# Kernel tuning notes

Measured on AMD Instinct MI355X. Metric: run time of the kernel, lower is better.

## Reference

```python
import jax, jax.numpy as jnp
import numpy as np

N_NODES, N_RELS, D, DEG = 100000, 2000, 128, 16
N_EDGES = N_NODES * DEG


def setup_inputs() -> dict:
    key = jax.random.key(0)
    k1, k2, k3, k4, k5 = jax.random.split(key, 5)
    # subject column: sorted and covers every node (tf.math.segment_sum requires
    # sorted segment ids; full coverage avoids 0/0 in the normalization)
    subj = jnp.repeat(jnp.arange(N_NODES, dtype=jnp.int64), DEG)
    rel = jax.random.randint(k1, (N_EDGES,), 0, N_RELS, dtype=jnp.int64)
    obj = jax.random.randint(k2, (N_EDGES,), 0, N_NODES, dtype=jnp.int64)
    triples = jnp.stack([subj, rel, obj], axis=1)[None]  # [1, E, 3]
    features = jax.random.normal(k3, (N_NODES, D), jnp.float32)
    rel_emb = jax.random.normal(k4, (N_RELS, D), jnp.float32)
    attn_kernel = jax.random.normal(k5, (D, 1), jnp.float32) * 0.05  # keep exp() finite
    return {"triples": triples, "features": features, "rel_emb": rel_emb,
            "attn_kernel": attn_kernel}


def reference(triples, features, rel_emb, attn_kernel):
    # single head, 'concat' reduction, linear activation, no bias
    t = jnp.squeeze(triples, 0).astype(jnp.int32)  # [E, 3]
    subj, rel_idx, obj_idx = t[:, 0], t[:, 1], t[:, 2]
    n = features.shape[0]

    obj_embs = features[obj_idx]          # [E, D] gather
    edge_embs = rel_emb[rel_idx]          # [E, D] gather

    # tf.nn.l2_normalize(edge_embs, 1) with eps 1e-12
    edge_n = edge_embs * jax.lax.rsqrt(
        jnp.maximum(jnp.sum(edge_embs * edge_embs, axis=1, keepdims=True), 1e-12))
    # Householder-like reflection (note: projection onto normalized dir, scaled
    # by the UNnormalized edge embedding, exactly as in the source)
    refl = jnp.sum(obj_embs * edge_n, axis=1, keepdims=True) * edge_embs
    obj_embs = obj_embs - 2.0 * refl      # [E, D]

    # per-relation attention logit, gathered per edge
    att_value = jnp.exp(rel_emb @ attn_kernel)[rel_idx]  # [E, 1]

    num = jax.ops.segment_sum(att_value * obj_embs, subj, num_segments=n)  # [N, D]
    den = jax.ops.segment_sum(att_value, subj, num_segments=n)             # [N, 1]
    return num / den
```

## Files before the change

### kernel.cpp

```cpp
#include <hip/hip_runtime.h>
#include <hip/hip_fp16.h>

#define N_NODES 100000
#define N_RELS  2000
#define D       128
#define DEG     16

#define RELWS_BYTES  16384
#define FEAT16_BYTES ((size_t)N_NODES * D * 2)
#define REL16_BYTES  ((size_t)N_RELS * D * 2)
#define WS_NEED      (RELWS_BYTES + FEAT16_BYTES + REL16_BYTES)

static __device__ __forceinline__ __half2 bc_h2(unsigned int u) {
  return __builtin_bit_cast(__half2, u);
}
static __device__ __forceinline__ int bc_i(float f) {
  return __builtin_bit_cast(int, f);
}
static __device__ __forceinline__ float bc_f(int i) {
  return __builtin_bit_cast(float, i);
}

static __device__ __forceinline__ float row16_sum_bcast(float v) {
  v += bc_f(__builtin_amdgcn_update_dpp(0, bc_i(v), 0x111, 0xF, 0xF, false));
  v += bc_f(__builtin_amdgcn_update_dpp(0, bc_i(v), 0x112, 0xF, 0xF, false));
  v += bc_f(__builtin_amdgcn_update_dpp(0, bc_i(v), 0x114, 0xF, 0xF, false));
  v += bc_f(__builtin_amdgcn_update_dpp(0, bc_i(v), 0x118, 0xF, 0xF, false));
  return bc_f(__builtin_amdgcn_ds_swizzle(bc_i(v), 0x1F0));
}

__global__ __launch_bounds__(256) void rel_pre_kernel(
    const float* __restrict__ rel_emb,
    const float* __restrict__ attn,
    float2* __restrict__ relws,
    unsigned int* __restrict__ rel16u) {
  const int wave = threadIdx.x >> 6;
  const int lane = threadIdx.x & 63;
  const int r = blockIdx.x * 4 + wave;
  float2 ev = *(const float2*)(rel_emb + (size_t)r * D + lane * 2);
  float2 av = *(const float2*)(attn + lane * 2);
  rel16u[r * 64 + lane] =
      __builtin_bit_cast(unsigned int, __builtin_amdgcn_cvt_pkrtz(ev.x, ev.y));
  float ss = ev.x * ev.x + ev.y * ev.y;
  float dt = ev.x * av.x + ev.y * av.y;
#pragma unroll
  for (int off = 32; off >= 1; off >>= 1) {
    ss += __shfl_xor(ss, off, 64);
    dt += __shfl_xor(dt, off, 64);
  }
  if (lane == 0) {
    float inv = rsqrtf(fmaxf(ss, 1e-12f));
    relws[r] = make_float2(inv, expf(dt));
  }
}

__global__ __launch_bounds__(256) void cvt_f32_f16_kernel(
    const float* __restrict__ src, uint2* __restrict__ dst) {
  const int i = blockIdx.x * 256 + threadIdx.x;
  float4 v = ((const float4*)src)[i];
  uint2 o;
  o.x = __builtin_bit_cast(unsigned int, __builtin_amdgcn_cvt_pkrtz(v.x, v.y));
  o.y = __builtin_bit_cast(unsigned int, __builtin_amdgcn_cvt_pkrtz(v.z, v.w));
  dst[i] = o;
}

__global__ __launch_bounds__(256) void gat16_kernel(
    const int* __restrict__ triples,
    const unsigned short* __restrict__ feat16,
    const unsigned short* __restrict__ rel16,
    const float2* __restrict__ relws,
    float* __restrict__ out) {
  __shared__ uint2 recs[256];

  const int tid  = threadIdx.x;
  const int s    = tid & 15;
  const int g    = (tid >> 4) & 3;
  const int wave = tid >> 6;
  const int node = blockIdx.x * 16 + wave * 4 + g;

  const int* t = triples + (size_t)node * (DEG * 3);
  const int tr = t[3 * s + 1];
  const int to = t[3 * s + 2];
  const float2 ia = relws[tr];
  const float att = ia.y;
  const float cf  = 2.f * att * ia.x;

  float den = att;
  den += __shfl_xor(den, 1);
  den += __shfl_xor(den, 2);
  den += __shfl_xor(den, 4);
  den += __shfl_xor(den, 8);
  const float rden = 1.f / den;

  recs[tid] = make_uint2(
      (unsigned int)((to << 11) | tr),
      __builtin_bit_cast(unsigned int, __builtin_amdgcn_cvt_pkrtz(att, cf)));
  __syncthreads();

  const int rbase = tid & 0xF0;

  uint4 ofb[8], efb[8];
  unsigned int pacb[8];
#pragma unroll
  for (int i = 0; i < 8; ++i) {
    uint2 r = recs[rbase + i];
    pacb[i] = r.y;
    ofb[i] = *(const uint4*)(feat16 + (size_t)(r.x >> 11) * D + s * 8);
    efb[i] = *(const uint4*)(rel16 + (size_t)(r.x & 2047u) * D + s * 8);
  }

  __half2 acc1[4], acc2[4];
#pragma unroll
  for (int j = 0; j < 4; ++j) {
    acc1[j] = __float2half2_rn(0.f);
    acc2[j] = __float2half2_rn(0.f);
  }

#pragma unroll
  for (int i = 0; i < DEG; ++i) {
    const int j = i & 7;
    const uint4 of = ofb[j];
    const uint4 ef = efb[j];
    const unsigned int ac = pacb[j];
    if (i + 8 < DEG) {
      uint2 r = recs[rbase + i + 8];
      pacb[j] = r.y;
      ofb[j] = *(const uint4*)(feat16 + (size_t)(r.x >> 11) * D + s * 8);
      efb[j] = *(const uint4*)(rel16 + (size_t)(r.x & 2047u) * D + s * 8);
    }

    const __half2 o0 = bc_h2(of.x), o1 = bc_h2(of.y), o2 = bc_h2(of.z), o3 = bc_h2(of.w);
    const __half2 e0 = bc_h2(ef.x), e1 = bc_h2(ef.y), e2 = bc_h2(ef.z), e3 = bc_h2(ef.w);

    __half2 pp = __hmul2(o0, e0);
    pp = __hfma2(o1, e1, pp);
    pp = __hfma2(o2, e2, pp);
    pp = __hfma2(o3, e3, pp);
    const float pd = row16_sum_bcast(__low2float(pp) + __high2float(pp));

    const __half2 h = bc_h2(ac);
    const __half2 att2 = __half2half2(__low2half(h));
    const __half2 c2 = __float2half2_rn(__high2float(h) * pd);

    acc1[0] = __hfma2(att2, o0, acc1[0]);
    acc1[1] = __hfma2(att2, o1, acc1[1]);
    acc1[2] = __hfma2(att2, o2, acc1[2]);
    acc1[3] = __hfma2(att2, o3, acc1[3]);
    acc2[0] = __hfma2(c2, e0, acc2[0]);
    acc2[1] = __hfma2(c2, e1, acc2[1]);
    acc2[2] = __hfma2(c2, e2, acc2[2]);
    acc2[3] = __hfma2(c2, e3, acc2[3]);
  }

  float* op = out + (size_t)node * D + s * 8;
  float4 r0, r1;
  {
    float2 a0 = __half22float2(acc1[0]), b0 = __half22float2(acc2[0]);
    float2 a1 = __half22float2(acc1[1]), b1 = __half22float2(acc2[1]);
    r0.x = (a0.x - b0.x) * rden; r0.y = (a0.y - b0.y) * rden;
    r0.z = (a1.x - b1.x) * rden; r0.w = (a1.y - b1.y) * rden;
    float2 a2 = __half22float2(acc1[2]), b2 = __half22float2(acc2[2]);
    float2 a3 = __half22float2(acc1[3]), b3 = __half22float2(acc2[3]);
    r1.x = (a2.x - b2.x) * rden; r1.y = (a2.y - b2.y) * rden;
    r1.z = (a3.x - b3.x) * rden; r1.w = (a3.y - b3.y) * rden;
  }
  *(float4*)op = r0;
  *(float4*)(op + 4) = r1;
}

__global__ __launch_bounds__(256) void gat_kernel(
    const int* __restrict__ triples,
    const float* __restrict__ features,
    const float* __restrict__ rel_emb,
    const float2* __restrict__ relws,
    float* __restrict__ out) {
  const int wave = threadIdx.x >> 6;
  const int lane = threadIdx.x & 63;
  const int node = blockIdx.x * 4 + wave;
  const int* t = triples + (size_t)node * DEG * 3;
  int tv = (lane < DEG * 3) ? t[lane] : 0;
  float2 acc = make_float2(0.f, 0.f);
  float den = 0.f;
#pragma unroll
  for (int i = 0; i < DEG; ++i) {
    const int rel = __builtin_amdgcn_readfirstlane(__shfl(tv, 3 * i + 1, 64));
    const int obj = __builtin_amdgcn_readfirstlane(__shfl(tv, 3 * i + 2, 64));
    float2 ia = relws[rel];
    float2 ov = *(const float2*)(features + (size_t)obj * D + lane * 2);
    float2 ev = *(const float2*)(rel_emb + (size_t)rel * D + lane * 2);
    float pd = ov.x * ev.x + ov.y * ev.y;
#pragma unroll
    for (int off = 32; off >= 1; off >>= 1) pd += __shfl_xor(pd, off, 64);
    const float c = 2.f * pd * ia.x;
    const float att = ia.y;
    acc.x += att * (ov.x - c * ev.x);
    acc.y += att * (ov.y - c * ev.y);
    den += att;
  }
  const float r = 1.f / den;
  *(float2*)(out + (size_t)node * D + lane * 2) =
      make_float2(acc.x * r, acc.y * r);
}

extern "C" void kernel_launch(void* const* d_in, const int* in_sizes, int n_in,
                              void* d_out, int out_size, void* d_ws, size_t ws_size,
                              hipStream_t stream) {
  const int*   triples  = (const int*)d_in[0];
  const float* features = (const float*)d_in[1];
  const float* rel_emb  = (const float*)d_in[2];
  const float* attn     = (const float*)d_in[3];
  float*       out      = (float*)d_out;

  float2* relws = (float2*)d_ws;

  if (ws_size >= WS_NEED) {
    unsigned short* feat16 = (unsigned short*)((char*)d_ws + RELWS_BYTES);
    unsigned int*   rel16u = (unsigned int*)((char*)d_ws + RELWS_BYTES + FEAT16_BYTES);
    rel_pre_kernel<<<N_RELS / 4, 256, 0, stream>>>(rel_emb, attn, relws, rel16u);
    cvt_f32_f16_kernel<<<(N_NODES * D / 4) / 256, 256, 0, stream>>>(
        features, (uint2*)feat16);
    gat16_kernel<<<N_NODES / 16, 256, 0, stream>>>(
        triples, feat16, (const unsigned short*)rel16u, relws, out);
  } else {
    rel_pre_kernel<<<N_RELS / 4, 256, 0, stream>>>(rel_emb, attn, relws,
                                                   (unsigned int*)d_ws);
    gat_kernel<<<N_NODES / 4, 256, 0, stream>>>(
        triples, features, rel_emb, relws, out);
  }
}
```

Measured before the change: 173.0 us.

## Fuse preprocessing kernels and hand-schedule gather loads with inline asm waitcnts

Measured after the change: 169.4 us. 1.02x faster.

```diff
diff --git a/kernel.cpp b/kernel.cpp
--- a/kernel.cpp
+++ b/kernel.cpp
@@ -10,6 +10,8 @@
 #define FEAT16_BYTES ((size_t)N_NODES * D * 2)
 #define REL16_BYTES  ((size_t)N_RELS * D * 2)
 #define WS_NEED      (RELWS_BYTES + FEAT16_BYTES + REL16_BYTES)
+
+typedef unsigned int u32x4 __attribute__((ext_vector_type(4)));
 
 static __device__ __forceinline__ __half2 bc_h2(unsigned int u) {
   return __builtin_bit_cast(__half2, u);
@@ -27,6 +29,42 @@
   v += bc_f(__builtin_amdgcn_update_dpp(0, bc_i(v), 0x114, 0xF, 0xF, false));
   v += bc_f(__builtin_amdgcn_update_dpp(0, bc_i(v), 0x118, 0xF, 0xF, false));
   return bc_f(__builtin_amdgcn_ds_swizzle(bc_i(v), 0x1F0));
+}
+
+__global__ __launch_bounds__(256) void pre_kernel(
+    const float* __restrict__ features,
+    const float* __restrict__ rel_emb,
+    const float* __restrict__ attn,
+    float2* __restrict__ relws,
+    unsigned int* __restrict__ rel16u,
+    uint2* __restrict__ feat16v) {
+  const int i = blockIdx.x * 256 + threadIdx.x;
+  float4 v = ((const float4*)features)[i];
+  uint2 o;
+  o.x = __builtin_bit_cast(unsigned int, __builtin_amdgcn_cvt_pkrtz(v.x, v.y));
+  o.y = __builtin_bit_cast(unsigned int, __builtin_amdgcn_cvt_pkrtz(v.z, v.w));
+  feat16v[i] = o;
+
+  if (blockIdx.x < N_RELS / 4) {
+    const int wave = threadIdx.x >> 6;
+    const int lane = threadIdx.x & 63;
+    const int r = blockIdx.x * 4 + wave;
+    float2 ev = *(const float2*)(rel_emb + (size_t)r * D + lane * 2);
+    float2 av = *(const float2*)(attn + lane * 2);
+    rel16u[r * 64 + lane] =
+        __builtin_bit_cast(unsigned int, __builtin_amdgcn_cvt_pkrtz(ev.x, ev.y));
+    float ss = ev.x * ev.x + ev.y * ev.y;
+    float dt = ev.x * av.x + ev.y * av.y;
+#pragma unroll
+    for (int off = 32; off >= 1; off >>= 1) {
+      ss += __shfl_xor(ss, off, 64);
+      dt += __shfl_xor(dt, off, 64);
+    }
+    if (lane == 0) {
+      float inv = rsqrtf(fmaxf(ss, 1e-12f));
+      relws[r] = make_float2(inv, expf(dt));
+    }
+  }
 }
 
 __global__ __launch_bounds__(256) void rel_pre_kernel(
@@ -54,15 +92,50 @@
   }
 }
 
-__global__ __launch_bounds__(256) void cvt_f32_f16_kernel(
-    const float* __restrict__ src, uint2* __restrict__ dst) {
-  const int i = blockIdx.x * 256 + threadIdx.x;
-  float4 v = ((const float4*)src)[i];
-  uint2 o;
-  o.x = __builtin_bit_cast(unsigned int, __builtin_amdgcn_cvt_pkrtz(v.x, v.y));
-  o.y = __builtin_bit_cast(unsigned int, __builtin_amdgcn_cvt_pkrtz(v.z, v.w));
-  dst[i] = o;
-}
+
+#define GAT_WAIT(n) asm volatile("s_waitcnt vmcnt(" #n ")")
+
+#define GAT_ISSUE(slot, rx)                                                    \
+  {                                                                            \
+    const unsigned long long fo_ =                                             \
+        (unsigned long long)(feat16 + (size_t)((rx) >> 11) * D + s * 8);       \
+    const unsigned long long fe_ =                                             \
+        (unsigned long long)(rel16 + (size_t)((rx) & 2047u) * D + s * 8);      \
+    asm volatile("global_load_dwordx4 %0, %1, off"                             \
+                 : "=v"(ofb[(slot)]) : "v"(fo_));                              \
+    asm volatile("global_load_dwordx4 %0, %1, off"                             \
+                 : "=v"(efb[(slot)]) : "v"(fe_));                              \
+  }
+
+#define GAT_ITER(i, vmw)                                                       \
+  {                                                                            \
+    GAT_WAIT(vmw);                                                             \
+    __builtin_amdgcn_sched_barrier(0);                                         \
+    const u32x4 of = ofb[(i) & 7];                                             \
+    const u32x4 ef = efb[(i) & 7];                                             \
+    const unsigned int ac = rc[(i)].y;                                         \
+    if constexpr ((i) + 8 < DEG) GAT_ISSUE((i) & 7, rc[(i) + 8].x);            \
+    const __half2 o0 = bc_h2(of.x), o1 = bc_h2(of.y), o2 = bc_h2(of.z),        \
+                  o3 = bc_h2(of.w);                                            \
+    const __half2 e0 = bc_h2(ef.x), e1 = bc_h2(ef.y), e2 = bc_h2(ef.z),        \
+                  e3 = bc_h2(ef.w);                                            \
+    __half2 pp = __hmul2(o0, e0);                                              \
+    pp = __hfma2(o1, e1, pp);                                                  \
+    pp = __hfma2(o2, e2, pp);                                                  \
+    pp = __hfma2(o3, e3, pp);                                                  \
+    const float pd = row16_sum_bcast(__low2float(pp) + __high2float(pp));      \
+    const __half2 h = bc_h2(ac);                                               \
+    const __half2 att2 = __half2half2(__low2half(h));                          \
+    const __half2 c2 = __float2half2_rn(__high2float(h) * pd);                 \
+    acc1[0] = __hfma2(att2, o0, acc1[0]);                                      \
+    acc1[1] = __hfma2(att2, o1, acc1[1]);                                      \
+    acc1[2] = __hfma2(att2, o2, acc1[2]);                                      \
+    acc1[3] = __hfma2(att2, o3, acc1[3]);                                      \
+    acc2[0] = __hfma2(c2, e0, acc2[0]);                                        \
+    acc2[1] = __hfma2(c2, e1, acc2[1]);                                        \
+    acc2[2] = __hfma2(c2, e2, acc2[2]);                                        \
+    acc2[3] = __hfma2(c2, e3, acc2[3]);                                        \
+  }
 
 __global__ __launch_bounds__(256) void gat16_kernel(
     const int* __restrict__ triples,
@@ -99,15 +172,14 @@
 
   const int rbase = tid & 0xF0;
 
-  uint4 ofb[8], efb[8];
-  unsigned int pacb[8];
-#pragma unroll
-  for (int i = 0; i < 8; ++i) {
-    uint2 r = recs[rbase + i];
-    pacb[i] = r.y;
-    ofb[i] = *(const uint4*)(feat16 + (size_t)(r.x >> 11) * D + s * 8);
-    efb[i] = *(const uint4*)(rel16 + (size_t)(r.x & 2047u) * D + s * 8);
-  }
+  uint2 rc[16];
+#pragma unroll
+  for (int i = 0; i < 16; ++i) rc[i] = recs[rbase + i];
+
+  u32x4 ofb[8], efb[8];
+  GAT_WAIT(0);
+#pragma unroll
+  for (int i = 0; i < 8; ++i) GAT_ISSUE(i, rc[i].x);
 
   __half2 acc1[4], acc2[4];
 #pragma unroll
@@ -116,41 +188,10 @@
     acc2[j] = __float2half2_rn(0.f);
   }
 
-#pragma unroll
-  for (int i = 0; i < DEG; ++i) {
-    const int j = i & 7;
-    const uint4 of = ofb[j];
-    const uint4 ef = efb[j];
-    const unsigned int ac = pacb[j];
-    if (i + 8 < DEG) {
-      uint2 r = recs[rbase + i + 8];
-      pacb[j] = r.y;
-      ofb[j] = *(const uint4*)(feat16 + (size_t)(r.x >> 11) * D + s * 8);
-      efb[j] = *(const uint4*)(rel16 + (size_t)(r.x & 2047u) * D + s * 8);
-    }
-
-    const __half2 o0 = bc_h2(of.x), o1 = bc_h2(of.y), o2 = bc_h2(of.z), o3 = bc_h2(of.w);
-    const __half2 e0 = bc_h2(ef.x), e1 = bc_h2(ef.y), e2 = bc_h2(ef.z), e3 = bc_h2(ef.w);
-
-    __half2 pp = __hmul2(o0, e0);
-    pp = __hfma2(o1, e1, pp);
-    pp = __hfma2(o2, e2, pp);
-    pp = __hfma2(o3, e3, pp);
-    const float pd = row16_sum_bcast(__low2float(pp) + __high2float(pp));
-
-    const __half2 h = bc_h2(ac);
-    const __half2 att2 = __half2half2(__low2half(h));
-    const __half2 c2 = __float2half2_rn(__high2float(h) * pd);
-
-    acc1[0] = __hfma2(att2, o0, acc1[0]);
-    acc1[1] = __hfma2(att2, o1, acc1[1]);
-    acc1[2] = __hfma2(att2, o2, acc1[2]);
-    acc1[3] = __hfma2(att2, o3, acc1[3]);
-    acc2[0] = __hfma2(c2, e0, acc2[0]);
-    acc2[1] = __hfma2(c2, e1, acc2[1]);
-    acc2[2] = __hfma2(c2, e2, acc2[2]);
-    acc2[3] = __hfma2(c2, e3, acc2[3]);
-  }
+  GAT_ITER(0, 14)  GAT_ITER(1, 14)  GAT_ITER(2, 14)  GAT_ITER(3, 14)
+  GAT_ITER(4, 14)  GAT_ITER(5, 14)  GAT_ITER(6, 14)  GAT_ITER(7, 14)
+  GAT_ITER(8, 14)  GAT_ITER(9, 12)  GAT_ITER(10, 10) GAT_ITER(11, 8)
+  GAT_ITER(12, 6)  GAT_ITER(13, 4)  GAT_ITER(14, 2)  GAT_ITER(15, 0)
 
   float* op = out + (size_t)node * D + s * 8;
   float4 r0, r1;
@@ -216,9 +257,8 @@
   if (ws_size >= WS_NEED) {
     unsigned short* feat16 = (unsigned short*)((char*)d_ws + RELWS_BYTES);
     unsigned int*   rel16u = (unsigned int*)((char*)d_ws + RELWS_BYTES + FEAT16_BYTES);
-    rel_pre_kernel<<<N_RELS / 4, 256, 0, stream>>>(rel_emb, attn, relws, rel16u);
-    cvt_f32_f16_kernel<<<(N_NODES * D / 4) / 256, 256, 0, stream>>>(
-        features, (uint2*)feat16);
+    pre_kernel<<<(N_NODES * D / 4) / 256, 256, 0, stream>>>(
+        features, rel_emb, attn, relws, rel16u, (uint2*)feat16);
     gat16_kernel<<<N_NODES / 16, 256, 0, stream>>>(
         triples, feat16, (const unsigned short*)rel16u, relws, out);
   } else {
```
